# Kernel optimization log

Hardware: AMD Instinct MI355X
Metric: run time of the kernel (lower is better)

The kernel has to match this reference:

```python
import jax, jax.numpy as jnp
import numpy as np

N_NODES = 10000
N_EDGES = 640000
D = 128
BN_EPS = 1e-5


def setup_inputs() -> dict:
    key = jax.random.key(0)
    k1, k2, k3 = jax.random.split(key, 3)
    x = jax.random.normal(k1, (N_NODES, D), dtype=jnp.float32)
    edge_index = jax.random.randint(k2, (2, N_EDGES), 0, N_NODES, dtype=jnp.int64)
    W = jax.random.normal(k3, (D, D), dtype=jnp.float32) * (1.0 / np.sqrt(D))
    b = jnp.zeros((D,), dtype=jnp.float32)
    gamma = jnp.ones((D,), dtype=jnp.float32)
    beta = jnp.zeros((D,), dtype=jnp.float32)
    return {"x": x, "edge_index": edge_index, "W": W, "b": b, "gamma": gamma, "beta": beta}


def reference(x, edge_index, W, b, gamma, beta):
    # GINConv: out_i = MLP((1+eps)*x_i + sum_{j->i} x_j), eps=0
    src = edge_index[0]
    dst = edge_index[1]
    agg = jax.ops.segment_sum(x[src], dst, num_segments=N_NODES)  # [N, D]
    h = agg + x  # (1 + eps) * x with eps = 0
    # MLP inside GINConv: Linear + ReLU
    h = jnp.maximum(h @ W + b, 0.0)
    # outer F.relu (idempotent after inner ReLU, kept for faithfulness)
    h = jnp.maximum(h, 0.0)
    # BatchNorm1d, training-mode batch statistics (biased variance)
    mean = jnp.mean(h, axis=0)
    var = jnp.var(h, axis=0)
    h = (h - mean) * jax.lax.rsqrt(var + BN_EPS) * gamma + beta
    # Dropout in eval mode -> identity. his_x = [h]; return the main output.
    return h
```

## Files before the change

kernel.cpp:

```cpp
#include <hip/hip_runtime.h>

#define N_NODES 10000
#define N_EDGES 640000
#define D 128
#define BN_EPS 1e-5f
#define CAP 128
#define NSTRIPE 16
#define RPB 8
#define NB 1250
#define BCAP 704
#define ABLK 256
#define ASLICE 2500
#define CSENT 1250

typedef _Float16 half8_t __attribute__((ext_vector_type(8)));
typedef float f32x4 __attribute__((ext_vector_type(4)));
typedef unsigned short u16;

__global__ __launch_bounds__(256) void k_bin(
    const int* __restrict__ ei,
    const float4* __restrict__ x4,
    int* cur,
    int* __restrict__ recs,
    half8_t* __restrict__ xh)
{
    __shared__ int cnt[NB];
    __shared__ int base[NB];
    const int b = blockIdx.x, t = threadIdx.x;

    {
        const int n8 = N_NODES * D / 8;
        for (int i = b * 256 + t; i < n8; i += ABLK * 256) {
            const float4 a = x4[2 * i];
            const float4 c = x4[2 * i + 1];
            half8_t h;
            h[0] = (_Float16)a.x; h[1] = (_Float16)a.y;
            h[2] = (_Float16)a.z; h[3] = (_Float16)a.w;
            h[4] = (_Float16)c.x; h[5] = (_Float16)c.y;
            h[6] = (_Float16)c.z; h[7] = (_Float16)c.w;
            xh[i] = h;
        }
    }

    for (int i = t; i < NB; i += 256) cnt[i] = 0;
    __syncthreads();

    const int e0 = b * ASLICE;
    for (int i = t; i < ASLICE; i += 256)
        atomicAdd(&cnt[ei[N_EDGES + e0 + i] >> 3], 1);
    __syncthreads();

    const unsigned cbase = (unsigned)cur[CSENT];
    for (int i = t; i < NB; i += 256) {
        const int c = cnt[i];
        base[i] = (int)((unsigned)atomicAdd(&cur[i], c) - cbase);
        cnt[i] = 0;
    }
    __syncthreads();

    for (int i = t; i < ASLICE; i += 256) {
        const int e = e0 + i;
        const int d = ei[N_EDGES + e];
        const int s = ei[e];
        const int bin = d >> 3;
        const int p = base[bin] + atomicAdd(&cnt[bin], 1);
        if (p < BCAP) recs[bin * BCAP + p] = (s << 3) | (d & 7);
    }
}

__global__ __launch_bounds__(256) void k_gfill(
    const float* __restrict__ x,
    const half8_t* __restrict__ xh8,
    const int* __restrict__ cur,
    const int* __restrict__ recs,
    const float* __restrict__ W,
    const float* __restrict__ bias,
    float* __restrict__ out,
    float* __restrict__ stats)
{
    __shared__ u16 lst[RPB * CAP];
    __shared__ int cnt[RPB];
    __shared__ float hs[RPB][D];
    const int tid  = threadIdx.x;
    const int bin  = blockIdx.x;
    const int wv   = tid >> 6;
    const int lane = tid & 63;
    const int qq   = lane >> 4;
    const int l    = lane & 15;
    const float4* __restrict__ x4 = (const float4*)x;

    if (tid < RPB) cnt[tid] = 0;
    __syncthreads();

    const unsigned cbase = (unsigned)cur[CSENT];
    int nrec = (int)((unsigned)cur[bin] - cbase);
    if (nrec > BCAP) nrec = BCAP;
    const int* __restrict__ br = recs + bin * BCAP;
    for (int i = tid; i < nrec; i += 256) {
        const int r = __builtin_nontemporal_load(&br[i]);
        const int p = atomicAdd(&cnt[r & 7], 1);
        if (p < CAP) lst[(r & 7) * CAP + p] = (u16)(r >> 3);
    }
    __syncthreads();

    #pragma unroll
    for (int j = 0; j < 2; j++) {
        const int lrow = wv * 2 + j;
        const int node = bin * RPB + lrow;
        int n = cnt[lrow];
        if (n > CAP) n = CAP;
        const u16* __restrict__ myl = &lst[lrow * CAP];
        float acc[8];
        #pragma unroll
        for (int z = 0; z < 8; z++) acc[z] = 0.f;

        int i = 0;
        for (; i + 64 <= n; i += 64) {
            const int sj = (int)myl[i + lane];
            #pragma unroll
            for (int b = 0; b < 2; b++) {
                half8_t v[8];
                #pragma unroll
                for (int u = 0; u < 8; u++) {
                    const int s = __shfl(sj, 4 * (b * 8 + u) + qq, 64);
                    v[u] = xh8[(size_t)s * 16 + l];
                }
                #pragma unroll
                for (int u = 0; u < 8; u++)
                    #pragma unroll
                    for (int z = 0; z < 8; z++)
                        acc[z] += (float)v[u][z];
            }
        }
        const int c = n - i;
        if (c > 0) {
            const int sj = (lane < c) ? (int)myl[i + lane] : 0;
            const int quads = c >> 2;
            for (int t2 = 0; t2 < quads; t2 += 8) {
                half8_t v[8];
                #pragma unroll
                for (int u = 0; u < 8; u++) {
                    const int s = __shfl(sj, (4 * (t2 + u) + qq) & 63, 64);
                    v[u] = xh8[(size_t)s * 16 + l];
                }
                #pragma unroll
                for (int u = 0; u < 8; u++) {
                    if (t2 + u < quads) {
                        #pragma unroll
                        for (int z = 0; z < 8; z++)
                            acc[z] += (float)v[u][z];
                    }
                }
            }
            const int r = c & 3;
            if (r > 0) {
                const int s = __shfl(sj, (4 * quads + qq) & 63, 64);
                const half8_t vv = xh8[(size_t)s * 16 + l];
                if (qq < r) {
                    #pragma unroll
                    for (int z = 0; z < 8; z++)
                        acc[z] += (float)vv[z];
                }
            }
        }
        #pragma unroll
        for (int z = 0; z < 8; z++) {
            acc[z] += __shfl_xor(acc[z], 16, 64);
            acc[z] += __shfl_xor(acc[z], 32, 64);
        }
        if (qq == 0) {
            const float4 xa = x4[(size_t)node * 32 + 2 * l];
            const float4 xb = x4[(size_t)node * 32 + 2 * l + 1];
            *(float4*)&hs[lrow][8 * l] =
                make_float4(acc[0] + xa.x, acc[1] + xa.y, acc[2] + xa.z, acc[3] + xa.w);
            *(float4*)&hs[lrow][8 * l + 4] =
                make_float4(acc[4] + xb.x, acc[5] + xb.y, acc[6] + xb.z, acc[7] + xb.w);
        }
    }
    __syncthreads();

    const int col = tid & 127;
    const int rg  = tid >> 7;
    float a[4] = {0.f, 0.f, 0.f, 0.f};
    #pragma unroll 8
    for (int k = 0; k < D; k++) {
        const float w = W[k * D + col];
        #pragma unroll
        for (int r = 0; r < 4; r++)
            a[r] = fmaf(hs[rg * 4 + r][k], w, a[r]);
    }

    const float bcol = bias[col];
    float s1 = 0.f, s2 = 0.f;
    #pragma unroll
    for (int r = 0; r < 4; r++) {
        const float v = fmaxf(a[r] + bcol, 0.f);
        __builtin_nontemporal_store(v, &out[(size_t)(bin * RPB + rg * 4 + r) * D + col]);
        s1 += v;
        s2 += v * v;
    }

    __syncthreads();
    float* red = &hs[0][0];
    red[tid]       = s1;
    red[256 + tid] = s2;
    __syncthreads();
    if (tid < D) {
        float* sp = &stats[(size_t)(bin & (NSTRIPE - 1)) * 256];
        atomicAdd(&sp[tid],     red[tid]       + red[tid + 128]);
        atomicAdd(&sp[D + tid], red[256 + tid] + red[256 + tid + 128]);
    }
}

__global__ __launch_bounds__(256) void k_bn(
    float* out,
    const float* __restrict__ stats,
    const float* __restrict__ gamma,
    const float* __restrict__ beta)
{
    __shared__ float sc[D], sh[D];
    const int tid = threadIdx.x;
    if (tid < D) {
        const float fbase = stats[NSTRIPE * 256];
        float s = 0.f, q = 0.f;
        #pragma unroll
        for (int cp = 0; cp < NSTRIPE; cp++) {
            s += stats[cp * 256 + tid]     - fbase;
            q += stats[cp * 256 + D + tid] - fbase;
        }
        const float mean = s * (1.0f / N_NODES);
        const float var  = q * (1.0f / N_NODES) - mean * mean;
        const float scale = gamma[tid] * rsqrtf(var + BN_EPS);
        sc[tid] = scale;
        sh[tid] = beta[tid] - mean * scale;
    }
    __syncthreads();

    f32x4* o4 = (f32x4*)out;
    #pragma unroll
    for (int j = 0; j < 2; j++) {
        const int f = blockIdx.x * 512 + j * 256 + tid;
        const int c = (f & 31) << 2;
        f32x4 v = __builtin_nontemporal_load(&o4[f]);
        v.x = v.x * sc[c]     + sh[c];
        v.y = v.y * sc[c + 1] + sh[c + 1];
        v.z = v.z * sc[c + 2] + sh[c + 2];
        v.w = v.w * sc[c + 3] + sh[c + 3];
        __builtin_nontemporal_store(v, &o4[f]);
    }
}

extern "C" void kernel_launch(void* const* d_in, const int* in_sizes, int n_in,
                              void* d_out, int out_size, void* d_ws, size_t ws_size,
                              hipStream_t stream)
{
    const float* x     = (const float*)d_in[0];
    const int*   ei    = (const int*)d_in[1];
    const float* W     = (const float*)d_in[2];
    const float* bias  = (const float*)d_in[3];
    const float* gamma = (const float*)d_in[4];
    const float* beta  = (const float*)d_in[5];
    float* out = (float*)d_out;

    float*   stats = (float*)d_ws;
    int*     cur   = (int*)(stats + NSTRIPE * 256 + 8);
    int*     recs  = cur + 1280;
    half8_t* xh    = (half8_t*)(recs + NB * BCAP);

    k_bin<<<ABLK, 256, 0, stream>>>(ei, (const float4*)x, cur, recs, xh);
    k_gfill<<<NB, 256, 0, stream>>>(x, xh, cur, recs, W, bias, out, stats);
    k_bn<<<N_NODES * D / 2048, 256, 0, stream>>>(out, stats, gamma, beta);
}
```

Baseline: 117.1 us.

## Coarsen edge bins to 64 nodes with local sort for coalesced record writes

The binning kernel now groups edges into 157 coarse bins of 64 destination nodes. Each block counting-sorts its slice in shared memory, then writes each bin's records contiguously to global memory, replacing scattered per-edge writes across 1250 small bins. The gather kernel reads the whole coarse bin (about 4096 records) and keeps only those matching its 8-node sub-bin. That means every coarse bin is read eight times, and per-block shared memory and scan synchronization go up.

After: 116.6 us. No clear change (-0.4%).

```diff
diff --git a/kernel.cpp b/kernel.cpp
--- a/kernel.cpp
+++ b/kernel.cpp
@@ -8,7 +8,8 @@
 #define NSTRIPE 16
 #define RPB 8
 #define NB 1250
-#define BCAP 704
+#define NBC 157
+#define BCAPC 4608
 #define ABLK 256
 #define ASLICE 2500
 #define CSENT 1250
@@ -24,8 +25,11 @@
     int* __restrict__ recs,
     half8_t* __restrict__ xh)
 {
-    __shared__ int cnt[NB];
-    __shared__ int base[NB];
+    __shared__ int cnt[NBC];
+    __shared__ int base_[NBC];
+    __shared__ int loff[NBC];
+    __shared__ int sc[256];
+    __shared__ int sorted[ASLICE];
     const int b = blockIdx.x, t = threadIdx.x;
 
     {
@@ -42,19 +46,29 @@
         }
     }
 
-    for (int i = t; i < NB; i += 256) cnt[i] = 0;
+    if (t < NBC) cnt[t] = 0;
     __syncthreads();
 
     const int e0 = b * ASLICE;
     for (int i = t; i < ASLICE; i += 256)
-        atomicAdd(&cnt[ei[N_EDGES + e0 + i] >> 3], 1);
-    __syncthreads();
+        atomicAdd(&cnt[ei[N_EDGES + e0 + i] >> 6], 1);
+    __syncthreads();
+
+    sc[t] = (t < NBC) ? cnt[t] : 0;
+    __syncthreads();
+    #pragma unroll
+    for (int off = 1; off < 256; off <<= 1) {
+        const int add = (t >= off) ? sc[t - off] : 0;
+        __syncthreads();
+        sc[t] += add;
+        __syncthreads();
+    }
 
     const unsigned cbase = (unsigned)cur[CSENT];
-    for (int i = t; i < NB; i += 256) {
-        const int c = cnt[i];
-        base[i] = (int)((unsigned)atomicAdd(&cur[i], c) - cbase);
-        cnt[i] = 0;
+    if (t < NBC) {
+        loff[t]  = sc[t] - cnt[t];
+        base_[t] = (int)((unsigned)atomicAdd(&cur[t], cnt[t]) - cbase);
+        cnt[t]   = 0;
     }
     __syncthreads();
 
@@ -62,9 +76,21 @@
         const int e = e0 + i;
         const int d = ei[N_EDGES + e];
         const int s = ei[e];
-        const int bin = d >> 3;
-        const int p = base[bin] + atomicAdd(&cnt[bin], 1);
-        if (p < BCAP) recs[bin * BCAP + p] = (s << 3) | (d & 7);
+        const int bin = d >> 6;
+        const int p = atomicAdd(&cnt[bin], 1);
+        sorted[loff[bin] + p] = (s << 6) | (d & 63);
+    }
+    __syncthreads();
+
+    const int g = t >> 4, sl = t & 15;
+    for (int bin = g; bin < NBC; bin += 16) {
+        const int c  = cnt[bin];
+        const int gb = base_[bin];
+        const int lo = loff[bin];
+        for (int k = sl; k < c; k += 16) {
+            const int pos = gb + k;
+            if (pos < BCAPC) recs[bin * BCAPC + pos] = sorted[lo + k];
+        }
     }
 }
 
@@ -83,6 +109,8 @@
     __shared__ float hs[RPB][D];
     const int tid  = threadIdx.x;
     const int bin  = blockIdx.x;
+    const int cb   = bin >> 3;
+    const int sub  = bin & 7;
     const int wv   = tid >> 6;
     const int lane = tid & 63;
     const int qq   = lane >> 4;
@@ -93,13 +121,15 @@
     __syncthreads();
 
     const unsigned cbase = (unsigned)cur[CSENT];
-    int nrec = (int)((unsigned)cur[bin] - cbase);
-    if (nrec > BCAP) nrec = BCAP;
-    const int* __restrict__ br = recs + bin * BCAP;
+    int nrec = (int)((unsigned)cur[cb] - cbase);
+    if (nrec > BCAPC) nrec = BCAPC;
+    const int* __restrict__ br = recs + cb * BCAPC;
     for (int i = tid; i < nrec; i += 256) {
-        const int r = __builtin_nontemporal_load(&br[i]);
-        const int p = atomicAdd(&cnt[r & 7], 1);
-        if (p < CAP) lst[(r & 7) * CAP + p] = (u16)(r >> 3);
+        const int r = br[i];
+        if (((r >> 3) & 7) == sub) {
+            const int p = atomicAdd(&cnt[r & 7], 1);
+            if (p < CAP) lst[(r & 7) * CAP + p] = (u16)(r >> 6);
+        }
     }
     __syncthreads();
 
@@ -265,7 +295,7 @@
     float*   stats = (float*)d_ws;
     int*     cur   = (int*)(stats + NSTRIPE * 256 + 8);
     int*     recs  = cur + 1280;
-    half8_t* xh    = (half8_t*)(recs + NB * BCAP);
+    half8_t* xh    = (half8_t*)(recs + NBC * BCAPC);
 
     k_bin<<<ABLK, 256, 0, stream>>>(ei, (const float4*)x, cur, recs, xh);
     k_gfill<<<NB, 256, 0, stream>>>(x, xh, cur, recs, W, bias, out, stats);
```
